# Optimization experiments

Measured on AMD Instinct MI355X. Metric: run time of the kernel, lower is better.

## Reference

```python
import jax, jax.numpy as jnp
import numpy as np

B, N, D_IN, D_OUT, H = 8, 1024, 768, 768, 12
D_HEAD = D_OUT // H  # 64; per-head softmax scale is sqrt(D_HEAD)


def setup_inputs() -> dict:
    key = jax.random.key(0)
    kx, kq, kk, kv, kwo, kbo = jax.random.split(key, 6)
    s_in = 1.0 / np.sqrt(D_IN)
    s_out = 1.0 / np.sqrt(D_OUT)
    return {
        "x": jax.random.normal(kx, (B, N, D_IN), dtype=jnp.float32),
        # stacked per-head Linear weights, torch layout [out, in] -> [H, d_head, D_IN]
        "Wq": jax.random.uniform(kq, (H, D_HEAD, D_IN), jnp.float32, -s_in, s_in),
        "Wk": jax.random.uniform(kk, (H, D_HEAD, D_IN), jnp.float32, -s_in, s_in),
        "Wv": jax.random.uniform(kv, (H, D_HEAD, D_IN), jnp.float32, -s_in, s_in),
        "Wo": jax.random.uniform(kwo, (D_OUT, D_OUT), jnp.float32, -s_out, s_out),
        "bo": jax.random.uniform(kbo, (D_OUT,), jnp.float32, -s_out, s_out),
    }


def reference(x, Wq, Wk, Wv, Wo, bo):
    # Per-head projections, batched over heads: [B, H, N, d_head]
    q = jnp.einsum('bnd,hed->bhne', x, Wq)
    k = jnp.einsum('bnd,hed->bhne', x, Wk)
    v = jnp.einsum('bnd,hed->bhne', x, Wv)
    scale = 1.0 / np.sqrt(D_HEAD)
    scores = jnp.einsum('bhie,bhje->bhij', q, k) * scale  # [B, H, N, N]
    att = jax.nn.softmax(scores, axis=-1)
    out = jnp.einsum('bhij,bhje->bhie', att, v)  # [B, H, N, d_head]
    # concat heads along last dim: [B, N, H*d_head]
    out = out.transpose(0, 2, 1, 3).reshape(B, N, D_OUT)
    return out @ Wo.T + bo
```

## Files before the change

### kernel.cpp

```cpp
#include <hip/hip_runtime.h>
#include <hip/hip_bf16.h>


typedef unsigned short u16;
typedef unsigned int u32;
typedef __attribute__((ext_vector_type(8))) short bf8;
typedef __attribute__((ext_vector_type(4))) short bf4;
typedef __attribute__((ext_vector_type(4))) float f4;
typedef __attribute__((ext_vector_type(4))) unsigned short us4;

#define NB 8
#define NSEQ 1024
#define DMODEL 768
#define NHEAD 12
#define DHEAD 64

#define XELEMS   (NB * NSEQ * DMODEL)
#define WELEMS   (DMODEL * DMODEL)

__device__ __forceinline__ float b2f(u16 u) {
  union { unsigned int i; float f; } c; c.i = ((unsigned int)u) << 16; return c.f;
}
__device__ __forceinline__ u16 f2b(float f) {
  union { float f; unsigned int i; } c; c.f = f;
  unsigned int r = c.i + 0x7fffu + ((c.i >> 16) & 1u);
  return (u16)(r >> 16);
}
__device__ __forceinline__ void gl_lds16(const u16* g, u16* l) {
  __builtin_amdgcn_global_load_lds(
      (const __attribute__((address_space(1))) unsigned int*)g,
      (__attribute__((address_space(3))) unsigned int*)l, 16, 0, 0);
}

struct CvtArgs {
  const float* src[5];
  u16* dst[5];
};
#define G0 (XELEMS / 4)
#define GW (WELEMS / 4)
#define GTOT (G0 + 4 * GW)

__global__ __launch_bounds__(256) void cvt_kernel(CvtArgs a) {
  size_t g = (size_t)blockIdx.x * 256 + threadIdx.x;
  if (g >= GTOT) return;
  int t; size_t off;
  if (g < G0) { t = 0; off = g; }
  else { size_t r = g - G0; t = 1 + (int)(r / GW); off = r % GW; }
  f4 v = *(const f4*)(a.src[t] + off * 4);
  us4 o;
  o[0] = f2b(v[0]); o[1] = f2b(v[1]); o[2] = f2b(v[2]); o[3] = f2b(v[3]);
  *(us4*)(a.dst[t] + off * 4) = o;
}

__global__ __launch_bounds__(512, 2) void qkv_gemm(
    const u16* __restrict__ x, const u16* __restrict__ Wq,
    const u16* __restrict__ Wk, const u16* __restrict__ Wv,
    u16* __restrict__ q, u16* __restrict__ k, u16* __restrict__ vt)
{
  __shared__ __align__(16) u16 lA[3][256 * 64];
  __shared__ __align__(16) u16 lB[3][128 * 64];

  const int tid  = threadIdx.x;
  const int lane = tid & 63;
  const int w    = tid >> 6;
  const int wm4  = w >> 1;
  const int wn2  = w & 1;
  const int col  = lane & 15;
  const int quad = lane >> 4;

  const int bid = blockIdx.x;
  const int wg  = (bid & 7) * 72 + (bid >> 3);
  const int bm  = wg / 18;
  const int bn  = wg % 18;

  const int m0 = bm * 256;
  const int proj = bn / 6;
  const u16* Wsel = (proj == 0) ? Wq : (proj == 1 ? Wk : Wv);
  const int nrem0 = (bn % 6) * 128;

  const int srow8 = lane >> 3;
  const int sg    = (lane & 7) ^ srow8;

  const u16* gA = x    + (size_t)(m0    + w * 8 + srow8) * DMODEL + sg * 8;
  const u16* gB = Wsel + (size_t)(nrem0 + w * 8 + srow8) * DMODEL + sg * 8;

  f4 acc[4][4];
#pragma unroll
  for (int i = 0; i < 4; i++)
#pragma unroll
    for (int j = 0; j < 4; j++) acc[i][j] = (f4)0.0f;

#define QKV_STAGE(T, BUF)                                                      \
  do {                                                                         \
    const int kk_ = (T) * 64;                                                  \
    _Pragma("unroll")                                                          \
    for (int r_ = 0; r_ < 4; r_++)                                             \
      gl_lds16(gA + (size_t)r_ * 64 * DMODEL + kk_,                            \
               &lA[BUF][(r_ * 64 + w * 8) * 64]);                              \
    _Pragma("unroll")                                                          \
    for (int r_ = 0; r_ < 2; r_++)                                             \
      gl_lds16(gB + (size_t)r_ * 64 * DMODEL + kk_,                            \
               &lB[BUF][(r_ * 64 + w * 8) * 64]);                              \
  } while (0)

  QKV_STAGE(0, 0);
  QKV_STAGE(1, 1);

  for (int t = 0; t < 12; t++) {
    if (t < 11) { asm volatile("s_waitcnt vmcnt(6)" ::: "memory"); }
    else        { asm volatile("s_waitcnt vmcnt(0)" ::: "memory"); }
    __builtin_amdgcn_s_barrier();
    asm volatile("" ::: "memory");

    if (t < 10) QKV_STAGE(t + 2, (t + 2) % 3);

    const int buf = t % 3;
    bf8 af[4][2], bfr[4][2];
#pragma unroll
    for (int mt = 0; mt < 4; mt++) {
      const int row = wm4 * 64 + mt * 16 + col;
#pragma unroll
      for (int kt = 0; kt < 2; kt++)
        af[mt][kt] = *(const bf8*)&lA[buf][row * 64 + (((kt * 4 + quad) ^ (row & 7)) << 3)];
    }
#pragma unroll
    for (int nt = 0; nt < 4; nt++) {
      const int row = wn2 * 64 + nt * 16 + col;
#pragma unroll
      for (int kt = 0; kt < 2; kt++)
        bfr[nt][kt] = *(const bf8*)&lB[buf][row * 64 + (((kt * 4 + quad) ^ (row & 7)) << 3)];
    }

    __builtin_amdgcn_s_setprio(1);
#pragma unroll
    for (int mt = 0; mt < 4; mt++)
#pragma unroll
      for (int nt = 0; nt < 4; nt++)
#pragma unroll
        for (int kt = 0; kt < 2; kt++)
          acc[mt][nt] = __builtin_amdgcn_mfma_f32_16x16x32_bf16(af[mt][kt], bfr[nt][kt], acc[mt][nt], 0, 0, 0);
    __builtin_amdgcn_s_setprio(0);
  }
#undef QKV_STAGE

  const int mw0 = m0 + wm4 * 64, nw0 = nrem0 + wn2 * 64;
  if (proj == 2) {
#pragma unroll
    for (int mt = 0; mt < 4; mt++) {
#pragma unroll
      for (int nt = 0; nt < 4; nt++) {
        const int nc = nw0 + nt * 16 + col;
        const int h = nc >> 6, e = nc & 63;
        const int t0 = mw0 + mt * 16 + quad * 4;
        const int b = t0 >> 10, tok0 = t0 & 1023;
        us4 pk;
#pragma unroll
        for (int r = 0; r < 4; r++) pk[r] = f2b(acc[mt][nt][r]);
        *(us4*)(vt + ((size_t)(b * NHEAD + h) * DHEAD + e) * NSEQ + tok0) = pk;
      }
    }
  } else {
    u16* dst = (proj == 0) ? q : k;
#pragma unroll
    for (int mt = 0; mt < 4; mt++) {
#pragma unroll
      for (int nt = 0; nt < 4; nt++) {
        const int nc = nw0 + nt * 16 + col;
        const int h = nc >> 6, e = nc & 63;
#pragma unroll
        for (int r = 0; r < 4; r++) {
          const int t = mw0 + mt * 16 + quad * 4 + r;
          const int b = t >> 10, tok = t & 1023;
          dst[((size_t)(b * NHEAD + h) * NSEQ + tok) * DHEAD + e] = f2b(acc[mt][nt][r]);
        }
      }
    }
  }
}

__global__ __launch_bounds__(256, 3) void attn_kernel(
    const u16* __restrict__ q, const u16* __restrict__ k,
    const u16* __restrict__ vt, u16* __restrict__ attn)
{
  __shared__ __align__(16) u16 ldsK[2][64 * 64];
  __shared__ __align__(16) u16 ldsV[2][64 * 64];
  __shared__ __align__(16) u16 ldsP[4][32][72];

  const int tid  = threadIdx.x;
  const int lane = tid & 63;
  const int w    = tid >> 6;
  const int col  = lane & 15;
  const int quad = lane >> 4;

  const int idx = blockIdx.x;
  const int bh = idx % 96, qc = idx / 96;
  const int b = bh / 12, h = bh % 12;

  const size_t head = ((size_t)b * NHEAD + h) * NSEQ * DHEAD;
  const int q0 = qc * 128 + w * 32;

  const int srow8 = lane >> 3;
  const int sg    = (lane & 7) ^ srow8;

  bf8 onesf;
#pragma unroll
  for (int j = 0; j < 8; j++) onesf[j] = (short)0x3F80;

  bf8 qf[2][2];
#pragma unroll
  for (int qt = 0; qt < 2; qt++)
#pragma unroll
    for (int kt = 0; kt < 2; kt++) {
      const int row = q0 + qt * 16 + col;
      bf8 t = *(const bf8*)(q + head + (size_t)row * DHEAD + kt * 32 + quad * 8);
#pragma unroll
      for (int j = 0; j < 8; j++) t[j] = (short)f2b(b2f((u16)t[j]) * 0.125f);
      qf[qt][kt] = t;
    }

  f4 lacc[2];
  f4 o[2][4];
#pragma unroll
  for (int mt = 0; mt < 2; mt++) {
    lacc[mt] = (f4)0.0f;
#pragma unroll
    for (int et = 0; et < 4; et++) o[mt][et] = (f4)0.0f;
  }

#pragma unroll
  for (int i = 0; i < 2; i++) {
    const int li = w * 2 + i;
    gl_lds16(k  + head + (size_t)(li * 8 + srow8) * DHEAD + sg * 8, &ldsK[0][li * 512]);
    gl_lds16(vt + head + (size_t)(li * 8 + srow8) * NSEQ + sg * 8,  &ldsV[0][li * 512]);
  }

  for (int t = 0; t < NSEQ / 64; t++) {
    const int cur = t & 1;
    __syncthreads();
    if (t < NSEQ / 64 - 1) {
      const int kb2 = (t + 1) * 64;
#pragma unroll
      for (int i = 0; i < 2; i++) {
        const int li = w * 2 + i;
        gl_lds16(k  + head + (size_t)(kb2 + li * 8 + srow8) * DHEAD + sg * 8,
                 &ldsK[cur ^ 1][li * 512]);
        gl_lds16(vt + head + (size_t)(li * 8 + srow8) * NSEQ + kb2 + sg * 8,
                 &ldsV[cur ^ 1][li * 512]);
      }
    }

    f4 st[4][2];
#pragma unroll
    for (int kvt = 0; kvt < 4; kvt++)
#pragma unroll
      for (int qt = 0; qt < 2; qt++) st[kvt][qt] = (f4)0.0f;
#pragma unroll
    for (int kt = 0; kt < 2; kt++) {
      bf8 kf[4];
#pragma unroll
      for (int kvt = 0; kvt < 4; kvt++) {
        const int row = kvt * 16 + col;
        kf[kvt] = *(const bf8*)&ldsK[cur][row * 64 + (((kt * 4 + quad) ^ (col & 7)) << 3)];
      }
      __builtin_amdgcn_s_setprio(1);
#pragma unroll
      for (int kvt = 0; kvt < 4; kvt++)
#pragma unroll
        for (int qt = 0; qt < 2; qt++)
          st[kvt][qt] = __builtin_amdgcn_mfma_f32_16x16x32_bf16(kf[kvt], qf[qt][kt], st[kvt][qt], 0, 0, 0);
      __builtin_amdgcn_s_setprio(0);
    }

#pragma unroll
    for (int kvt = 0; kvt < 4; kvt++)
#pragma unroll
      for (int qt = 0; qt < 2; qt++) {
        const f4 p = st[kvt][qt];
        bf4 pw;
        pw[0] = (short)f2b(__expf(p[0]));
        pw[1] = (short)f2b(__expf(p[1]));
        pw[2] = (short)f2b(__expf(p[2]));
        pw[3] = (short)f2b(__expf(p[3]));
        *(bf4*)&ldsP[w][qt * 16 + col][kvt * 16 + quad * 4] = pw;
      }
    asm volatile("" ::: "memory");

#pragma unroll
    for (int kt2 = 0; kt2 < 2; kt2++) {
      bf8 vf[4];
#pragma unroll
      for (int et = 0; et < 4; et++) {
        const int row = et * 16 + col;
        vf[et] = *(const bf8*)&ldsV[cur][row * 64 + (((kt2 * 4 + quad) ^ (col & 7)) << 3)];
      }
#pragma unroll
      for (int mt = 0; mt < 2; mt++) {
        const bf8 pf = *(const bf8*)&ldsP[w][mt * 16 + col][kt2 * 32 + quad * 8];
        __builtin_amdgcn_s_setprio(1);
        lacc[mt] = __builtin_amdgcn_mfma_f32_16x16x32_bf16(pf, onesf, lacc[mt], 0, 0, 0);
#pragma unroll
        for (int et = 0; et < 4; et++)
          o[mt][et] = __builtin_amdgcn_mfma_f32_16x16x32_bf16(pf, vf[et], o[mt][et], 0, 0, 0);
        __builtin_amdgcn_s_setprio(0);
      }
    }
  }

#pragma unroll
  for (int mt = 0; mt < 2; mt++)
#pragma unroll
    for (int r = 0; r < 4; r++) {
      const float inv = 1.0f / lacc[mt][r];
      const int token = q0 + mt * 16 + quad * 4 + r;
#pragma unroll
      for (int et = 0; et < 4; et++)
        attn[(size_t)(b * NSEQ + token) * DMODEL + h * DHEAD + et * 16 + col] =
            f2b(o[mt][et][r] * inv);
    }
}

__global__ __launch_bounds__(256, 4) void out_gemm(
    const u16* __restrict__ attn, const u16* __restrict__ Wo,
    const float* __restrict__ bo, float* __restrict__ out)
{
  __shared__ __align__(16) u16 lA[2][128 * 32];
  __shared__ __align__(16) u16 lB[2][128 * 32];

  const int tid  = threadIdx.x;
  const int lane = tid & 63;
  const int w    = tid >> 6;
  const int wm   = w >> 1, wn = w & 1;
  const int col  = lane & 15;
  const int quad = lane >> 4;
  const int bm = blockIdx.x;
  const int bn = blockIdx.y;

  const int m0 = bm * 128;
  const int n0 = bn * 128;

  const int srow = lane >> 2;
  const int sg   = (lane & 3) ^ ((srow >> 1) & 3);
  const u16* gA0 = attn + (size_t)(m0 + w * 32 + srow) * DMODEL + sg * 8;
  const u16* gB0 = Wo   + (size_t)(n0 + w * 32 + srow) * DMODEL + sg * 8;

  f4 acc[4][4];
#pragma unroll
  for (int i = 0; i < 4; i++)
#pragma unroll
    for (int j = 0; j < 4; j++) acc[i][j] = (f4)0.0f;

  gl_lds16(gA0, &lA[0][(w * 32) * 32]);
  gl_lds16(gA0 + (size_t)16 * DMODEL, &lA[0][(w * 32 + 16) * 32]);
  gl_lds16(gB0, &lB[0][(w * 32) * 32]);
  gl_lds16(gB0 + (size_t)16 * DMODEL, &lB[0][(w * 32 + 16) * 32]);

  for (int it = 0; it < 24; it++) {
    const int cur = it & 1;
    __syncthreads();
    if (it < 23) {
      const int kk = (it + 1) * 32;
      gl_lds16(gA0 + kk, &lA[cur ^ 1][(w * 32) * 32]);
      gl_lds16(gA0 + (size_t)16 * DMODEL + kk, &lA[cur ^ 1][(w * 32 + 16) * 32]);
      gl_lds16(gB0 + kk, &lB[cur ^ 1][(w * 32) * 32]);
      gl_lds16(gB0 + (size_t)16 * DMODEL + kk, &lB[cur ^ 1][(w * 32 + 16) * 32]);
    }

    bf8 af[4], bfr[4];
#pragma unroll
    for (int mt = 0; mt < 4; mt++) {
      const int row = wm * 64 + mt * 16 + col;
      af[mt] = *(const bf8*)&lA[cur][row * 32 + ((quad ^ ((row >> 1) & 3)) << 3)];
    }
#pragma unroll
    for (int nt = 0; nt < 4; nt++) {
      const int row = wn * 64 + nt * 16 + col;
      bfr[nt] = *(const bf8*)&lB[cur][row * 32 + ((quad ^ ((row >> 1) & 3)) << 3)];
    }
#pragma unroll
    for (int mt = 0; mt < 4; mt++)
#pragma unroll
      for (int nt = 0; nt < 4; nt++)
        acc[mt][nt] = __builtin_amdgcn_mfma_f32_16x16x32_bf16(af[mt], bfr[nt], acc[mt][nt], 0, 0, 0);
  }

  const int mw0 = m0 + wm * 64, nw0 = n0 + wn * 64;
#pragma unroll
  for (int mt = 0; mt < 4; mt++)
#pragma unroll
    for (int nt = 0; nt < 4; nt++) {
      const int n = nw0 + nt * 16 + col;
      const float bias = bo[n];
#pragma unroll
      for (int r = 0; r < 4; r++) {
        const int row = mw0 + mt * 16 + quad * 4 + r;
        out[(size_t)row * DMODEL + n] = acc[mt][nt][r] + bias;
      }
    }
}

extern "C" void kernel_launch(void* const* d_in, const int* in_sizes, int n_in,
                              void* d_out, int out_size, void* d_ws, size_t ws_size,
                              hipStream_t stream) {
  const float* x  = (const float*)d_in[0];
  const float* Wq = (const float*)d_in[1];
  const float* Wk = (const float*)d_in[2];
  const float* Wv = (const float*)d_in[3];
  const float* Wo = (const float*)d_in[4];
  const float* bo = (const float*)d_in[5];
  float* out = (float*)d_out;

  u16* xb   = (u16*)d_ws;
  u16* wqb  = xb  + XELEMS;
  u16* wkb  = wqb + WELEMS;
  u16* wvb  = wkb + WELEMS;
  u16* wob  = wvb + WELEMS;
  u16* q    = wob + WELEMS;
  u16* k    = q   + XELEMS;
  u16* vt   = k   + XELEMS;
  u16* attn = vt  + XELEMS;

  CvtArgs ca;
  ca.src[0] = x;  ca.src[1] = Wq;  ca.src[2] = Wk;  ca.src[3] = Wv;  ca.src[4] = Wo;
  ca.dst[0] = xb; ca.dst[1] = wqb; ca.dst[2] = wkb; ca.dst[3] = wvb; ca.dst[4] = wob;

  cvt_kernel<<<dim3((GTOT + 255) / 256), 256, 0, stream>>>(ca);
  qkv_gemm<<<dim3(576), 512, 0, stream>>>(xb, wqb, wkb, wvb, q, k, vt);
  attn_kernel<<<dim3(768), 256, 0, stream>>>(q, k, vt, attn);
  out_gemm<<<dim3(64, 6), 256, 0, stream>>>(attn, wob, bo, out);
}
```

Before: 188.5 us.

## Widen QKV GEMM tile to 256x192 with double buffering and fewer blocks

Changes the QKV projection GEMM tile from 256x128 to 256x192, so each warp holds a 4x6 accumulator grid and the grid shrinks from 576 to 384 blocks (one wave on 256 CUs with 2 blocks each is closer). The 3-stage LDS pipeline with explicit vmcnt waits becomes a 2-stage double buffer guarded by __syncthreads, and the k-loop is restructured so fragments load per k-subtile. The goal is more reuse of each A tile and fewer x re-reads. In exchange it gives up prefetch depth and setprio, and it raises register pressure.

```diff
diff --git a/kernel.cpp b/kernel.cpp
--- a/kernel.cpp
+++ b/kernel.cpp
@@ -57,8 +57,8 @@
     const u16* __restrict__ Wk, const u16* __restrict__ Wv,
     u16* __restrict__ q, u16* __restrict__ k, u16* __restrict__ vt)
 {
-  __shared__ __align__(16) u16 lA[3][256 * 64];
-  __shared__ __align__(16) u16 lB[3][128 * 64];
+  __shared__ __align__(16) u16 lA[2][256 * 64];
+  __shared__ __align__(16) u16 lB[2][192 * 64];
 
   const int tid  = threadIdx.x;
   const int lane = tid & 63;
@@ -69,86 +69,75 @@
   const int quad = lane >> 4;
 
   const int bid = blockIdx.x;
-  const int wg  = (bid & 7) * 72 + (bid >> 3);
-  const int bm  = wg / 18;
-  const int bn  = wg % 18;
+  const int wg  = (bid & 7) * 48 + (bid >> 3);
+  const int bm  = wg / 12;
+  const int bn  = wg % 12;
 
   const int m0 = bm * 256;
-  const int proj = bn / 6;
+  const int proj = bn >> 2;
   const u16* Wsel = (proj == 0) ? Wq : (proj == 1 ? Wk : Wv);
-  const int nrem0 = (bn % 6) * 128;
+  const int nrem0 = (bn & 3) * 192;
 
   const int srow8 = lane >> 3;
   const int sg    = (lane & 7) ^ srow8;
 
-  const u16* gA = x    + (size_t)(m0    + w * 8 + srow8) * DMODEL + sg * 8;
-  const u16* gB = Wsel + (size_t)(nrem0 + w * 8 + srow8) * DMODEL + sg * 8;
-
-  f4 acc[4][4];
+  const u16* gA = x    + (size_t)(m0    + srow8) * DMODEL + sg * 8;
+  const u16* gB = Wsel + (size_t)(nrem0 + srow8) * DMODEL + sg * 8;
+
+  f4 acc[4][6];
 #pragma unroll
   for (int i = 0; i < 4; i++)
 #pragma unroll
-    for (int j = 0; j < 4; j++) acc[i][j] = (f4)0.0f;
+    for (int j = 0; j < 6; j++) acc[i][j] = (f4)0.0f;
 
 #define QKV_STAGE(T, BUF)                                                      \
   do {                                                                         \
     const int kk_ = (T) * 64;                                                  \
     _Pragma("unroll")                                                          \
-    for (int r_ = 0; r_ < 4; r_++)                                             \
-      gl_lds16(gA + (size_t)r_ * 64 * DMODEL + kk_,                            \
-               &lA[BUF][(r_ * 64 + w * 8) * 64]);                              \
+    for (int i_ = 0; i_ < 4; i_++)                                             \
+      gl_lds16(gA + (size_t)(w * 32 + i_ * 8) * DMODEL + kk_,                  \
+               &lA[BUF][(w * 32 + i_ * 8) * 64]);                              \
     _Pragma("unroll")                                                          \
-    for (int r_ = 0; r_ < 2; r_++)                                             \
-      gl_lds16(gB + (size_t)r_ * 64 * DMODEL + kk_,                            \
-               &lB[BUF][(r_ * 64 + w * 8) * 64]);                              \
+    for (int j_ = 0; j_ < 3; j_++)                                             \
+      gl_lds16(gB + (size_t)(w * 24 + j_ * 8) * DMODEL + kk_,                  \
+               &lB[BUF][(w * 24 + j_ * 8) * 64]);                              \
   } while (0)
 
   QKV_STAGE(0, 0);
-  QKV_STAGE(1, 1);
 
   for (int t = 0; t < 12; t++) {
-    if (t < 11) { asm volatile("s_waitcnt vmcnt(6)" ::: "memory"); }
-    else        { asm volatile("s_waitcnt vmcnt(0)" ::: "memory"); }
-    __builtin_amdgcn_s_barrier();
-    asm volatile("" ::: "memory");
-
-    if (t < 10) QKV_STAGE(t + 2, (t + 2) % 3);
-
-    const int buf = t % 3;
-    bf8 af[4][2], bfr[4][2];
+    const int cur = t & 1;
+    __syncthreads();
+    if (t < 11) QKV_STAGE(t + 1, cur ^ 1);
+
+#pragma unroll
+    for (int kt = 0; kt < 2; kt++) {
+      bf8 af[4], bfr[6];
+#pragma unroll
+      for (int mt = 0; mt < 4; mt++) {
+        const int row = wm4 * 64 + mt * 16 + col;
+        af[mt] = *(const bf8*)&lA[cur][row * 64 + (((kt * 4 + quad) ^ (row & 7)) << 3)];
+      }
+#pragma unroll
+      for (int nt = 0; nt < 6; nt++) {
+        const int row = wn2 * 96 + nt * 16 + col;
+        bfr[nt] = *(const bf8*)&lB[cur][row * 64 + (((kt * 4 + quad) ^ (row & 7)) << 3)];
+      }
+#pragma unroll
+      for (int mt = 0; mt < 4; mt++)
+#pragma unroll
+        for (int nt = 0; nt < 6; nt++)
+          acc[mt][nt] = __builtin_amdgcn_mfma_f32_16x16x32_bf16(af[mt], bfr[nt], acc[mt][nt], 0, 0, 0);
+    }
+  }
+#undef QKV_STAGE
+
+  const int mw0 = m0 + wm4 * 64, nw0 = nrem0 + wn2 * 96;
+  if (proj == 2) {
 #pragma unroll
     for (int mt = 0; mt < 4; mt++) {
-      const int row = wm4 * 64 + mt * 16 + col;
-#pragma unroll
-      for (int kt = 0; kt < 2; kt++)
-        af[mt][kt] = *(const bf8*)&lA[buf][row * 64 + (((kt * 4 + quad) ^ (row & 7)) << 3)];
-    }
-#pragma unroll
-    for (int nt = 0; nt < 4; nt++) {
-      const int row = wn2 * 64 + nt * 16 + col;
-#pragma unroll
-      for (int kt = 0; kt < 2; kt++)
-        bfr[nt][kt] = *(const bf8*)&lB[buf][row * 64 + (((kt * 4 + quad) ^ (row & 7)) << 3)];
-    }
-
-    __builtin_amdgcn_s_setprio(1);
-#pragma unroll
-    for (int mt = 0; mt < 4; mt++)
-#pragma unroll
-      for (int nt = 0; nt < 4; nt++)
-#pragma unroll
-        for (int kt = 0; kt < 2; kt++)
-          acc[mt][nt] = __builtin_amdgcn_mfma_f32_16x16x32_bf16(af[mt][kt], bfr[nt][kt], acc[mt][nt], 0, 0, 0);
-    __builtin_amdgcn_s_setprio(0);
-  }
-#undef QKV_STAGE
-
-  const int mw0 = m0 + wm4 * 64, nw0 = nrem0 + wn2 * 64;
-  if (proj == 2) {
-#pragma unroll
-    for (int mt = 0; mt < 4; mt++) {
-#pragma unroll
-      for (int nt = 0; nt < 4; nt++) {
+#pragma unroll
+      for (int nt = 0; nt < 6; nt++) {
         const int nc = nw0 + nt * 16 + col;
         const int h = nc >> 6, e = nc & 63;
         const int t0 = mw0 + mt * 16 + quad * 4;
@@ -164,7 +153,7 @@
 #pragma unroll
     for (int mt = 0; mt < 4; mt++) {
 #pragma unroll
-      for (int nt = 0; nt < 4; nt++) {
+      for (int nt = 0; nt < 6; nt++) {
         const int nc = nw0 + nt * 16 + col;
         const int h = nc >> 6, e = nc & 63;
 #pragma unroll
@@ -424,7 +413,7 @@
   ca.dst[0] = xb; ca.dst[1] = wqb; ca.dst[2] = wkb; ca.dst[3] = wvb; ca.dst[4] = wob;
 
   cvt_kernel<<<dim3((GTOT + 255) / 256), 256, 0, stream>>>(ca);
-  qkv_gemm<<<dim3(576), 512, 0, stream>>>(xb, wqb, wkb, wvb, q, k, vt);
+  qkv_gemm<<<dim3(384), 512, 0, stream>>>(xb, wqb, wkb, wvb, q, k, vt);
   attn_kernel<<<dim3(768), 256, 0, stream>>>(q, k, vt, attn);
   out_gemm<<<dim3(64, 6), 256, 0, stream>>>(attn, wob, bo, out);
 }
```

Measured after the change: 191.0 us. About the same (+1.3%).

## Restructure output GEMM with 256x128 tiles, triple-buffered K=64 stages, XCD remap

Applied to the files above, without the earlier changes.

The output projection GEMM now uses 512-thread blocks computing 256x128 tiles with K-step 64. It triple-buffers LDS and uses explicit vmcnt waits plus raw barriers so two stages of loads are in flight during compute. It also remaps block IDs to group tiles per XCD, swaps the LDS swizzle to an 8-way XOR, and raises wave priority around the MFMA section. This aims to cut per-iteration sync overhead and memory latency stalls, at the cost of more LDS (144KB per block), lower occupancy and only 192 blocks.

```diff
diff --git a/kernel.cpp b/kernel.cpp
--- a/kernel.cpp
+++ b/kernel.cpp
@@ -319,29 +319,34 @@
     }
 }
 
-__global__ __launch_bounds__(256, 4) void out_gemm(
+__global__ __launch_bounds__(512, 2) void out_gemm(
     const u16* __restrict__ attn, const u16* __restrict__ Wo,
     const float* __restrict__ bo, float* __restrict__ out)
 {
-  __shared__ __align__(16) u16 lA[2][128 * 32];
-  __shared__ __align__(16) u16 lB[2][128 * 32];
+  __shared__ __align__(16) u16 lA[3][256 * 64];
+  __shared__ __align__(16) u16 lB[3][128 * 64];
 
   const int tid  = threadIdx.x;
   const int lane = tid & 63;
   const int w    = tid >> 6;
-  const int wm   = w >> 1, wn = w & 1;
+  const int wm4  = w >> 1;
+  const int wn2  = w & 1;
   const int col  = lane & 15;
   const int quad = lane >> 4;
-  const int bm = blockIdx.x;
-  const int bn = blockIdx.y;
-
-  const int m0 = bm * 128;
+
+  const int bid = blockIdx.x;
+  const int wg  = (bid & 7) * 24 + (bid >> 3);
+  const int bm  = wg / 6;
+  const int bn  = wg % 6;
+
+  const int m0 = bm * 256;
   const int n0 = bn * 128;
 
-  const int srow = lane >> 2;
-  const int sg   = (lane & 3) ^ ((srow >> 1) & 3);
-  const u16* gA0 = attn + (size_t)(m0 + w * 32 + srow) * DMODEL + sg * 8;
-  const u16* gB0 = Wo   + (size_t)(n0 + w * 32 + srow) * DMODEL + sg * 8;
+  const int srow8 = lane >> 3;
+  const int sg    = (lane & 7) ^ srow8;
+
+  const u16* gA = attn + (size_t)(m0 + w * 8 + srow8) * DMODEL + sg * 8;
+  const u16* gB = Wo   + (size_t)(n0 + w * 8 + srow8) * DMODEL + sg * 8;
 
   f4 acc[4][4];
 #pragma unroll
@@ -349,41 +354,60 @@
 #pragma unroll
     for (int j = 0; j < 4; j++) acc[i][j] = (f4)0.0f;
 
-  gl_lds16(gA0, &lA[0][(w * 32) * 32]);
-  gl_lds16(gA0 + (size_t)16 * DMODEL, &lA[0][(w * 32 + 16) * 32]);
-  gl_lds16(gB0, &lB[0][(w * 32) * 32]);
-  gl_lds16(gB0 + (size_t)16 * DMODEL, &lB[0][(w * 32 + 16) * 32]);
-
-  for (int it = 0; it < 24; it++) {
-    const int cur = it & 1;
-    __syncthreads();
-    if (it < 23) {
-      const int kk = (it + 1) * 32;
-      gl_lds16(gA0 + kk, &lA[cur ^ 1][(w * 32) * 32]);
-      gl_lds16(gA0 + (size_t)16 * DMODEL + kk, &lA[cur ^ 1][(w * 32 + 16) * 32]);
-      gl_lds16(gB0 + kk, &lB[cur ^ 1][(w * 32) * 32]);
-      gl_lds16(gB0 + (size_t)16 * DMODEL + kk, &lB[cur ^ 1][(w * 32 + 16) * 32]);
-    }
-
-    bf8 af[4], bfr[4];
+#define OUT_STAGE(T, BUF)                                                      \
+  do {                                                                         \
+    const int kk_ = (T) * 64;                                                  \
+    _Pragma("unroll")                                                          \
+    for (int r_ = 0; r_ < 4; r_++)                                             \
+      gl_lds16(gA + (size_t)r_ * 64 * DMODEL + kk_,                            \
+               &lA[BUF][(r_ * 64 + w * 8) * 64]);                              \
+    _Pragma("unroll")                                                          \
+    for (int r_ = 0; r_ < 2; r_++)                                             \
+      gl_lds16(gB + (size_t)r_ * 64 * DMODEL + kk_,                            \
+               &lB[BUF][(r_ * 64 + w * 8) * 64]);                              \
+  } while (0)
+
+  OUT_STAGE(0, 0);
+  OUT_STAGE(1, 1);
+
+  for (int t = 0; t < 12; t++) {
+    if (t < 11) { asm volatile("s_waitcnt vmcnt(6)" ::: "memory"); }
+    else        { asm volatile("s_waitcnt vmcnt(0)" ::: "memory"); }
+    __builtin_amdgcn_s_barrier();
+    asm volatile("" ::: "memory");
+
+    if (t < 10) OUT_STAGE(t + 2, (t + 2) % 3);
+
+    const int buf = t % 3;
+    bf8 af[4][2], bfr[4][2];
 #pragma unroll
     for (int mt = 0; mt < 4; mt++) {
-      const int row = wm * 64 + mt * 16 + col;
-      af[mt] = *(const bf8*)&lA[cur][row * 32 + ((quad ^ ((row >> 1) & 3)) << 3)];
+      const int row = wm4 * 64 + mt * 16 + col;
+#pragma unroll
+      for (int kt = 0; kt < 2; kt++)
+        af[mt][kt] = *(const bf8*)&lA[buf][row * 64 + (((kt * 4 + quad) ^ (row & 7)) << 3)];
     }
 #pragma unroll
     for (int nt = 0; nt < 4; nt++) {
-      const int row = wn * 64 + nt * 16 + col;
-      bfr[nt] = *(const bf8*)&lB[cur][row * 32 + ((quad ^ ((row >> 1) & 3)) << 3)];
-    }
+      const int row = wn2 * 64 + nt * 16 + col;
+#pragma unroll
+      for (int kt = 0; kt < 2; kt++)
+        bfr[nt][kt] = *(const bf8*)&lB[buf][row * 64 + (((kt * 4 + quad) ^ (row & 7)) << 3)];
+    }
+
+    __builtin_amdgcn_s_setprio(1);
 #pragma unroll
     for (int mt = 0; mt < 4; mt++)
 #pragma unroll
       for (int nt = 0; nt < 4; nt++)
-        acc[mt][nt] = __builtin_amdgcn_mfma_f32_16x16x32_bf16(af[mt], bfr[nt], acc[mt][nt], 0, 0, 0);
-  }
-
-  const int mw0 = m0 + wm * 64, nw0 = n0 + wn * 64;
+#pragma unroll
+        for (int kt = 0; kt < 2; kt++)
+          acc[mt][nt] = __builtin_amdgcn_mfma_f32_16x16x32_bf16(af[mt][kt], bfr[nt][kt], acc[mt][nt], 0, 0, 0);
+    __builtin_amdgcn_s_setprio(0);
+  }
+#undef OUT_STAGE
+
+  const int mw0 = m0 + wm4 * 64, nw0 = n0 + wn2 * 64;
 #pragma unroll
   for (int mt = 0; mt < 4; mt++)
 #pragma unroll
@@ -426,5 +450,5 @@
   cvt_kernel<<<dim3((GTOT + 255) / 256), 256, 0, stream>>>(ca);
   qkv_gemm<<<dim3(576), 512, 0, stream>>>(xb, wqb, wkb, wvb, q, k, vt);
   attn_kernel<<<dim3(768), 256, 0, stream>>>(q, k, vt, attn);
-  out_gemm<<<dim3(64, 6), 256, 0, stream>>>(attn, wob, bo, out);
-}
+  out_gemm<<<dim3(192), 512, 0, stream>>>(attn, wob, bo, out);
+}
```

Result: no change. 191.9 us (+1.8%).
